# Performance work log

Measured on AMD Instinct MI355X. Metric: run time of the kernel, lower is better.

The kernel has to match this reference:

```python
import jax, jax.numpy as jnp
import numpy as np

EPS = 1e-7
ROUTING_ITERS = 3

def squash(s, axis=-1):
    # v = (|s|^2 / (1+|s|^2)) * s / |s|
    sq = jnp.sum(jnp.square(s), axis=axis, keepdims=True)
    return (sq / (1.0 + sq)) * s / jnp.sqrt(sq + EPS)

def setup_inputs() -> dict:
    key = jax.random.key(0)
    k1, k2 = jax.random.split(key)
    B, NI, DI = 64, 2048, 8      # batch, input capsules, input capsule dim
    NC, DC = 32, 16              # output capsules, output capsule dim
    x = jax.random.normal(k1, (B, NI, DI), dtype=jnp.float32)
    W = jax.random.normal(k2, (NC, NI, DC, DI), dtype=jnp.float32) * 0.05
    return {"x": x, "W": W}

def reference(x, W):
    # x: [B, NI, DI], W: [NC, NI, DC, DI]
    # tf.einsum('iabc,abdc->iabd') == project each input capsule per output capsule
    u = jnp.einsum('bif,cidf->bcid', x, W)          # [B, NC, NI, DC]
    B, NC, NI, DC = u.shape
    b = jnp.zeros((B, NC, NI, 1), dtype=u.dtype)
    v = None
    for _ in range(ROUTING_ITERS):
        c = jax.nn.softmax(b, axis=1)                # coupling over output capsules
        s = jnp.sum(c * u, axis=2, keepdims=True)    # [B, NC, 1, DC]
        v = squash(s, axis=-1)                       # [B, NC, 1, DC]
        # original: reduce_sum(matmul(u, tile(v)^T), axis=3) == NI * <u_i, v>
        agree = jnp.sum(u * v, axis=-1, keepdims=True)  # [B, NC, NI, 1]
        b = b + NI * agree
    return jnp.squeeze(v, axis=2)                    # [B, NC, DC]
```

## Files before the change

### kernel.cpp

```cpp
#include <hip/hip_runtime.h>

#define NI 2048
#define NB 64
#define NC 32
#define DC 16
#define DI 8

static constexpr float SQ_EPS = 1e-7f;

typedef float f8 __attribute__((ext_vector_type(8)));

template <int MODE>
__global__
__attribute__((amdgpu_flat_work_group_size(512, 512), amdgpu_waves_per_eu(4, 4)))
void route_pass(
    const float* __restrict__ x, const float* __restrict__ W,
    const float* __restrict__ veff, float* __restrict__ partial)
{
    __shared__ float4 wbuf[4224];
    __shared__ float4 xbuf[128];

    const int tid   = threadIdx.x;
    const int wave  = tid >> 6;
    const int lane  = tid & 63;
    const int c     = lane & 31;
    const int dg    = lane >> 5;
    const int brel0 = wave * 2;
    const int b0    = blockIdx.y * 16 + brel0;

    f8 s0 = {};
    f8 s1 = {};

    f8 va = {}, vb = {};
    if (MODE == 1) {
        va = *reinterpret_cast<const f8*>(
            veff + (((size_t)b0 * 2 + dg) * 32 + c) * 8);
        vb = *reinterpret_cast<const f8*>(
            veff + (((size_t)(b0 + 1) * 2 + dg) * 32 + c) * 8);
    }

    for (int oct = 0; oct < 4; ++oct) {
        const int i0 = blockIdx.x * 16 + oct * 4;
        __syncthreads();
        {
            const int k   = tid & 31;
            const int p0  = tid >> 5;
            const int k10 = k & 15, kdg = k >> 4;
            for (int r = 0; r < 8; ++r) {
                const int p  = r * 16 + p0;
                const int cc = p >> 2;
                const int il = p & 3;
                wbuf[((il * 16 + k10) * 2 + kdg) * 33 + cc] =
                    reinterpret_cast<const float4*>(W)[
                        ((size_t)cc * NI + i0 + il) * 32 + k];
            }
        }
        if (tid < 128) {
            const int k    = tid & 7;
            const int brel = tid >> 3;
            xbuf[brel * 8 + k] = reinterpret_cast<const float4*>(x)[
                ((size_t)(blockIdx.y * 16 + brel) * NI + i0) * 2 + k];
        }
        __syncthreads();

        for (int il = 0; il < 4; ++il) {
            const float4 xa0 = xbuf[(brel0    ) * 8 + il * 2    ];
            const float4 xa1 = xbuf[(brel0    ) * 8 + il * 2 + 1];
            const float4 xc0 = xbuf[(brel0 + 1) * 8 + il * 2    ];
            const float4 xc1 = xbuf[(brel0 + 1) * 8 + il * 2 + 1];

            f8 u0 = {}, u1 = {};
#pragma unroll
            for (int dd = 0; dd < 8; ++dd) {
                const float4 wl = wbuf[((il * 16 + dd * 2    ) * 2 + dg) * 33 + c];
                const float4 wh = wbuf[((il * 16 + dd * 2 + 1) * 2 + dg) * 33 + c];
                u0[dd] = wl.x*xa0.x + wl.y*xa0.y + wl.z*xa0.z + wl.w*xa0.w
                       + wh.x*xa1.x + wh.y*xa1.y + wh.z*xa1.z + wh.w*xa1.w;
                u1[dd] = wl.x*xc0.x + wl.y*xc0.y + wl.z*xc0.z + wl.w*xc0.w
                       + wh.x*xc1.x + wh.y*xc1.y + wh.z*xc1.z + wh.w*xc1.w;
            }

            float c0, c1;
            if (MODE == 0) {
                c0 = c1 = 1.0f / 32.0f;
            } else {
                float a0 = 0.0f, a1 = 0.0f;
#pragma unroll
                for (int k = 0; k < 8; ++k) {
                    a0 += u0[k] * va[k];
                    a1 += u1[k] * vb[k];
                }
                a0 += __shfl_xor(a0, 32);
                a1 += __shfl_xor(a1, 32);
                float m0 = a0, m1 = a1;
#pragma unroll
                for (int off = 16; off >= 1; off >>= 1) {
                    m0 = fmaxf(m0, __shfl_xor(m0, off));
                    m1 = fmaxf(m1, __shfl_xor(m1, off));
                }
                const float e0 = __expf(a0 - m0);
                const float e1 = __expf(a1 - m1);
                float t0 = e0, t1 = e1;
#pragma unroll
                for (int off = 16; off >= 1; off >>= 1) {
                    t0 += __shfl_xor(t0, off);
                    t1 += __shfl_xor(t1, off);
                }
                c0 = e0 / t0;
                c1 = e1 / t1;
            }
            s0 += u0 * c0;
            s1 += u1 * c1;
        }
    }

    {
        const int pblk = blockIdx.y * gridDim.x + blockIdx.x;
        float* gp = partial +
            (((size_t)pblk * 16 + brel0) * 128 + dg * 64 + c * 2) * 4;
        *reinterpret_cast<f8*>(gp)       = s0;
        *reinterpret_cast<f8*>(gp + 512) = s1;
    }
}

__global__ __launch_bounds__(256) void reduce_squash(
    const float* __restrict__ partial, float* __restrict__ veff,
    float* __restrict__ out, int phase)
{
    const int gid = blockIdx.x * 256 + threadIdx.x;
    const int b   = gid >> 9;
    const int c   = (gid >> 4) & 31;
    const int d   = gid & 15;

    const float* pp = partial
        + ((size_t)(b >> 4) * 128 * 16 + (b & 15)) * 512
        + (d >> 3) * 256 + c * 8 + (d & 7);
    float v = 0.0f;
#pragma unroll 4
    for (int ib = 0; ib < 128; ++ib)
        v += pp[(size_t)ib * (16 * 512)];

    float sq = v * v;
#pragma unroll
    for (int off = 8; off >= 1; off >>= 1)
        sq += __shfl_xor(sq, off);
    const float scale = sq / ((1.0f + sq) * sqrtf(sq + SQ_EPS));

    if (phase == 3) {
        out[(b * NC + c) * DC + d] = scale * v;
    } else {
        const int idx = (((b * 2) + (d >> 3)) * 32 + c) * 8 + (d & 7);
        const float ns = scale * (float)NI * v;
        if (phase == 1) veff[idx] = ns;
        else            veff[idx] += ns;
    }
}

extern "C" void kernel_launch(void* const* d_in, const int* in_sizes, int n_in,
                              void* d_out, int out_size, void* d_ws, size_t ws_size,
                              hipStream_t stream) {
    (void)in_sizes; (void)n_in; (void)out_size; (void)ws_size;
    const float* x = (const float*)d_in[0];
    const float* W = (const float*)d_in[1];

    float* partial = (float*)d_ws;
    float* veff    = (float*)d_out;

    const dim3 grid(128, 4);

    route_pass<0><<<grid, 512, 0, stream>>>(x, W, nullptr, partial);
    reduce_squash<<<128, 256, 0, stream>>>(partial, veff, nullptr, 1);

    route_pass<1><<<grid, 512, 0, stream>>>(x, W, veff, partial);
    reduce_squash<<<128, 256, 0, stream>>>(partial, veff, nullptr, 2);

    route_pass<1><<<grid, 512, 0, stream>>>(x, W, veff, partial);
    reduce_squash<<<128, 256, 0, stream>>>(partial, nullptr, (float*)d_out, 3);
}
```

Measured before the change: 210.2 us.

## Process four batches per wave in routing pass and vectorize reduce kernel

Halves the routing block to 256 threads, with each wave handling four batch rows instead of two, so every W value read from LDS is reused across more batches. The softmax reduction now packs two batch rows into one shuffle chain by pairing half-waves, which cuts shuffle work. The reduce/squash kernel switches to one block per batch with float4 loads and stores, reducing load instruction count. The trade-off is more registers per thread and fewer waves per block, so there are fewer waves to hide latency.

New measurement: 201.2 us. 1.04x faster.

```diff
diff --git a/kernel.cpp b/kernel.cpp
--- a/kernel.cpp
+++ b/kernel.cpp
@@ -12,7 +12,7 @@
 
 template <int MODE>
 __global__
-__attribute__((amdgpu_flat_work_group_size(512, 512), amdgpu_waves_per_eu(4, 4)))
+__attribute__((amdgpu_flat_work_group_size(256, 256), amdgpu_waves_per_eu(2, 2)))
 void route_pass(
     const float* __restrict__ x, const float* __restrict__ W,
     const float* __restrict__ veff, float* __restrict__ partial)
@@ -25,29 +25,28 @@
     const int lane  = tid & 63;
     const int c     = lane & 31;
     const int dg    = lane >> 5;
-    const int brel0 = wave * 2;
+    const int brel0 = wave * 4;
     const int b0    = blockIdx.y * 16 + brel0;
 
-    f8 s0 = {};
-    f8 s1 = {};
+    f8 s0 = {}, s1 = {}, s2 = {}, s3 = {};
 
-    f8 va = {}, vb = {};
+    f8 va = {}, vb = {}, vc = {}, vd = {};
     if (MODE == 1) {
-        va = *reinterpret_cast<const f8*>(
-            veff + (((size_t)b0 * 2 + dg) * 32 + c) * 8);
-        vb = *reinterpret_cast<const f8*>(
-            veff + (((size_t)(b0 + 1) * 2 + dg) * 32 + c) * 8);
+        va = *reinterpret_cast<const f8*>(veff + (((size_t)(b0+0)*2 + dg)*32 + c)*8);
+        vb = *reinterpret_cast<const f8*>(veff + (((size_t)(b0+1)*2 + dg)*32 + c)*8);
+        vc = *reinterpret_cast<const f8*>(veff + (((size_t)(b0+2)*2 + dg)*32 + c)*8);
+        vd = *reinterpret_cast<const f8*>(veff + (((size_t)(b0+3)*2 + dg)*32 + c)*8);
     }
 
     for (int oct = 0; oct < 4; ++oct) {
         const int i0 = blockIdx.x * 16 + oct * 4;
         __syncthreads();
         {
-            const int k   = tid & 31;
-            const int p0  = tid >> 5;
+            const int k  = tid & 31;
+            const int p0 = tid >> 5;
             const int k10 = k & 15, kdg = k >> 4;
-            for (int r = 0; r < 8; ++r) {
-                const int p  = r * 16 + p0;
+            for (int r = 0; r < 16; ++r) {
+                const int p  = r * 8 + p0;
                 const int cc = p >> 2;
                 const int il = p & 3;
                 wbuf[((il * 16 + k10) * 2 + kdg) * 33 + cc] =
@@ -64,53 +63,62 @@
         __syncthreads();
 
         for (int il = 0; il < 4; ++il) {
-            const float4 xa0 = xbuf[(brel0    ) * 8 + il * 2    ];
-            const float4 xa1 = xbuf[(brel0    ) * 8 + il * 2 + 1];
-            const float4 xc0 = xbuf[(brel0 + 1) * 8 + il * 2    ];
-            const float4 xc1 = xbuf[(brel0 + 1) * 8 + il * 2 + 1];
+            const float4 xa0 = xbuf[(brel0+0)*8 + il*2], xa1 = xbuf[(brel0+0)*8 + il*2+1];
+            const float4 xb0 = xbuf[(brel0+1)*8 + il*2], xb1 = xbuf[(brel0+1)*8 + il*2+1];
+            const float4 xc0 = xbuf[(brel0+2)*8 + il*2], xc1 = xbuf[(brel0+2)*8 + il*2+1];
+            const float4 xd0 = xbuf[(brel0+3)*8 + il*2], xd1 = xbuf[(brel0+3)*8 + il*2+1];
 
-            f8 u0 = {}, u1 = {};
+            f8 u0 = {}, u1 = {}, u2 = {}, u3 = {};
 #pragma unroll
             for (int dd = 0; dd < 8; ++dd) {
-                const float4 wl = wbuf[((il * 16 + dd * 2    ) * 2 + dg) * 33 + c];
-                const float4 wh = wbuf[((il * 16 + dd * 2 + 1) * 2 + dg) * 33 + c];
+                const float4 wl = wbuf[((il*16 + dd*2    )*2 + dg)*33 + c];
+                const float4 wh = wbuf[((il*16 + dd*2 + 1)*2 + dg)*33 + c];
                 u0[dd] = wl.x*xa0.x + wl.y*xa0.y + wl.z*xa0.z + wl.w*xa0.w
                        + wh.x*xa1.x + wh.y*xa1.y + wh.z*xa1.z + wh.w*xa1.w;
-                u1[dd] = wl.x*xc0.x + wl.y*xc0.y + wl.z*xc0.z + wl.w*xc0.w
+                u1[dd] = wl.x*xb0.x + wl.y*xb0.y + wl.z*xb0.z + wl.w*xb0.w
+                       + wh.x*xb1.x + wh.y*xb1.y + wh.z*xb1.z + wh.w*xb1.w;
+                u2[dd] = wl.x*xc0.x + wl.y*xc0.y + wl.z*xc0.z + wl.w*xc0.w
                        + wh.x*xc1.x + wh.y*xc1.y + wh.z*xc1.z + wh.w*xc1.w;
+                u3[dd] = wl.x*xd0.x + wl.y*xd0.y + wl.z*xd0.z + wl.w*xd0.w
+                       + wh.x*xd1.x + wh.y*xd1.y + wh.z*xd1.z + wh.w*xd1.w;
             }
 
-            float c0, c1;
             if (MODE == 0) {
-                c0 = c1 = 1.0f / 32.0f;
+                const float cu = 1.0f / 32.0f;
+                s0 += u0 * cu; s1 += u1 * cu; s2 += u2 * cu; s3 += u3 * cu;
             } else {
-                float a0 = 0.0f, a1 = 0.0f;
 #pragma unroll
-                for (int k = 0; k < 8; ++k) {
-                    a0 += u0[k] * va[k];
-                    a1 += u1[k] * vb[k];
+                for (int pr = 0; pr < 2; ++pr) {
+                    const f8& ue = pr ? u2 : u0;
+                    const f8& uo = pr ? u3 : u1;
+                    const f8& ve = pr ? vc : va;
+                    const f8& vo = pr ? vd : vb;
+                    float pe = 0.0f, po = 0.0f;
+#pragma unroll
+                    for (int k = 0; k < 8; ++k) {
+                        pe += ue[k] * ve[k];
+                        po += uo[k] * vo[k];
+                    }
+                    const float send = (dg == 0) ? po : pe;
+                    const float recv = __shfl_xor(send, 32);
+                    float a = ((dg == 0) ? pe : po) + recv;
+                    float m = a;
+#pragma unroll
+                    for (int off = 16; off >= 1; off >>= 1)
+                        m = fmaxf(m, __shfl_xor(m, off));
+                    const float e = __expf(a - m);
+                    float t = e;
+#pragma unroll
+                    for (int off = 16; off >= 1; off >>= 1)
+                        t += __shfl_xor(t, off);
+                    const float mine  = e / t;
+                    const float other = __shfl_xor(mine, 32);
+                    const float ce = (dg == 0) ? mine : other;
+                    const float co = (dg == 0) ? other : mine;
+                    if (pr == 0) { s0 += u0 * ce; s1 += u1 * co; }
+                    else         { s2 += u2 * ce; s3 += u3 * co; }
                 }
-                a0 += __shfl_xor(a0, 32);
-                a1 += __shfl_xor(a1, 32);
-                float m0 = a0, m1 = a1;
-#pragma unroll
-                for (int off = 16; off >= 1; off >>= 1) {
-                    m0 = fmaxf(m0, __shfl_xor(m0, off));
-                    m1 = fmaxf(m1, __shfl_xor(m1, off));
-                }
-                const float e0 = __expf(a0 - m0);
-                const float e1 = __expf(a1 - m1);
-                float t0 = e0, t1 = e1;
-#pragma unroll
-                for (int off = 16; off >= 1; off >>= 1) {
-                    t0 += __shfl_xor(t0, off);
-                    t1 += __shfl_xor(t1, off);
-                }
-                c0 = e0 / t0;
-                c1 = e1 / t1;
             }
-            s0 += u0 * c0;
-            s1 += u1 * c1;
         }
     }
 
@@ -118,41 +126,50 @@
         const int pblk = blockIdx.y * gridDim.x + blockIdx.x;
         float* gp = partial +
             (((size_t)pblk * 16 + brel0) * 128 + dg * 64 + c * 2) * 4;
-        *reinterpret_cast<f8*>(gp)       = s0;
-        *reinterpret_cast<f8*>(gp + 512) = s1;
+        *reinterpret_cast<f8*>(gp)        = s0;
+        *reinterpret_cast<f8*>(gp +  512) = s1;
+        *reinterpret_cast<f8*>(gp + 1024) = s2;
+        *reinterpret_cast<f8*>(gp + 1536) = s3;
     }
 }
 
-__global__ __launch_bounds__(256) void reduce_squash(
+__global__ __launch_bounds__(128) void reduce_squash(
     const float* __restrict__ partial, float* __restrict__ veff,
     float* __restrict__ out, int phase)
 {
-    const int gid = blockIdx.x * 256 + threadIdx.x;
-    const int b   = gid >> 9;
-    const int c   = (gid >> 4) & 31;
-    const int d   = gid & 15;
+    const int b  = blockIdx.x;
+    const int c  = (threadIdx.x >> 2) & 31;
+    const int dq = threadIdx.x & 3;
 
-    const float* pp = partial
-        + ((size_t)(b >> 4) * 128 * 16 + (b & 15)) * 512
-        + (d >> 3) * 256 + c * 8 + (d & 7);
-    float v = 0.0f;
-#pragma unroll 4
-    for (int ib = 0; ib < 128; ++ib)
-        v += pp[(size_t)ib * (16 * 512)];
+    const float* base = partial
+        + ((size_t)(b >> 4) * 2048 + (b & 15)) * 512
+        + (dq >> 1) * 256 + c * 8 + (dq & 1) * 4;
+    float4 acc = make_float4(0.f, 0.f, 0.f, 0.f);
+#pragma unroll 8
+    for (int ib = 0; ib < 128; ++ib) {
+        const float4 p = *reinterpret_cast<const float4*>(base + (size_t)ib * 8192);
+        acc.x += p.x; acc.y += p.y; acc.z += p.z; acc.w += p.w;
+    }
 
-    float sq = v * v;
-#pragma unroll
-    for (int off = 8; off >= 1; off >>= 1)
-        sq += __shfl_xor(sq, off);
+    float sq = acc.x*acc.x + acc.y*acc.y + acc.z*acc.z + acc.w*acc.w;
+    sq += __shfl_xor(sq, 1);
+    sq += __shfl_xor(sq, 2);
     const float scale = sq / ((1.0f + sq) * sqrtf(sq + SQ_EPS));
 
     if (phase == 3) {
-        out[(b * NC + c) * DC + d] = scale * v;
+        float4* op = reinterpret_cast<float4*>(out + ((size_t)b * NC + c) * DC + dq * 4);
+        *op = make_float4(scale*acc.x, scale*acc.y, scale*acc.z, scale*acc.w);
     } else {
-        const int idx = (((b * 2) + (d >> 3)) * 32 + c) * 8 + (d & 7);
-        const float ns = scale * (float)NI * v;
-        if (phase == 1) veff[idx] = ns;
-        else            veff[idx] += ns;
+        const float ns = scale * (float)NI;
+        float4* vp = reinterpret_cast<float4*>(
+            veff + (((size_t)b * 2 + (dq >> 1)) * 32 + c) * 8 + (dq & 1) * 4);
+        if (phase == 1) {
+            *vp = make_float4(ns*acc.x, ns*acc.y, ns*acc.z, ns*acc.w);
+        } else {
+            float4 old = *vp;
+            *vp = make_float4(old.x + ns*acc.x, old.y + ns*acc.y,
+                              old.z + ns*acc.z, old.w + ns*acc.w);
+        }
     }
 }
 
@@ -168,12 +185,12 @@
 
     const dim3 grid(128, 4);
 
-    route_pass<0><<<grid, 512, 0, stream>>>(x, W, nullptr, partial);
-    reduce_squash<<<128, 256, 0, stream>>>(partial, veff, nullptr, 1);
+    route_pass<0><<<grid, 256, 0, stream>>>(x, W, nullptr, partial);
+    reduce_squash<<<64, 128, 0, stream>>>(partial, veff, nullptr, 1);
 
-    route_pass<1><<<grid, 512, 0, stream>>>(x, W, veff, partial);
-    reduce_squash<<<128, 256, 0, stream>>>(partial, veff, nullptr, 2);
+    route_pass<1><<<grid, 256, 0, stream>>>(x, W, veff, partial);
+    reduce_squash<<<64, 128, 0, stream>>>(partial, veff, nullptr, 2);
 
-    route_pass<1><<<grid, 512, 0, stream>>>(x, W, veff, partial);
-    reduce_squash<<<128, 256, 0, stream>>>(partial, nullptr, (float*)d_out, 3);
+    route_pass<1><<<grid, 256, 0, stream>>>(x, W, veff, partial);
+    reduce_squash<<<64, 128, 0, stream>>>(partial, nullptr, (float*)d_out, 3);
 }
```
